# Kernel optimization log

Measured on AMD Instinct MI355X. Metric: run time of the kernel, lower is better.

Reference implementation:

```python
import jax, jax.numpy as jnp
from jax import lax
import numpy as np

B = 8
NUM_ANCHORS = 1047552
PROPOSAL_COUNT = 1000
NMS_THRESHOLD = 0.7
RPN_BBOX_STD_DEV = np.array([0.1, 0.1, 0.2, 0.2], dtype=np.float32)
RPN_NMS_LIMIT = 6000


def setup_inputs() -> dict:
    key = jax.random.key(0)
    k1, k2, k3 = jax.random.split(key, 3)
    rpn_scores = jax.random.uniform(k1, (B, NUM_ANCHORS, 2), dtype=jnp.float32)
    rpn_bbox_delta = jax.random.normal(k2, (B, NUM_ANCHORS, 4), dtype=jnp.float32)
    # Build valid normalized anchors (y1,x1,y2,x2) from uniform randoms.
    u = jax.random.uniform(k3, (NUM_ANCHORS, 4), dtype=jnp.float32)
    cy, cx = u[:, 0], u[:, 1]
    h = u[:, 2] * 0.2 + 0.01
    w = u[:, 3] * 0.2 + 0.01
    anchors = jnp.stack([cy - 0.5 * h, cx - 0.5 * w, cy + 0.5 * h, cx + 0.5 * w], axis=-1)
    anchors = jnp.clip(anchors, 0.0, 1.0)
    return {"rpn_scores": rpn_scores, "rpn_bbox_delta": rpn_bbox_delta, "anchors": anchors}


def _apply_box_deltas(boxes, deltas):
    # boxes: [..., (y1,x1,y2,x2)], deltas: [..., (dy,dx,log(dh),log(dw))]
    h = boxes[..., 2] - boxes[..., 0]
    w = boxes[..., 3] - boxes[..., 1]
    cy = boxes[..., 0] + 0.5 * h + deltas[..., 0] * h
    cx = boxes[..., 1] + 0.5 * w + deltas[..., 1] * w
    h = h * jnp.exp(deltas[..., 2])
    w = w * jnp.exp(deltas[..., 3])
    y1 = cy - 0.5 * h
    x1 = cx - 0.5 * w
    return jnp.stack([y1, x1, y1 + h, x1 + w], axis=-1)


def _nms_indices(boxes):
    # Greedy NMS over boxes already sorted by descending score. boxes: [N,4].
    N = boxes.shape[0]
    areas = (boxes[:, 2] - boxes[:, 0]) * (boxes[:, 3] - boxes[:, 1])

    def body(i, state):
        valid, sel = state
        idx = jnp.argmax(valid)          # first still-valid box = highest score
        has = valid[idx]
        sel = sel.at[i].set(jnp.where(has, idx, -1))
        b = boxes[idx]
        yy1 = jnp.maximum(b[0], boxes[:, 0])
        xx1 = jnp.maximum(b[1], boxes[:, 1])
        yy2 = jnp.minimum(b[2], boxes[:, 2])
        xx2 = jnp.minimum(b[3], boxes[:, 3])
        inter = jnp.maximum(yy2 - yy1, 0.0) * jnp.maximum(xx2 - xx1, 0.0)
        union = areas[idx] + areas - inter
        iou = jnp.where(union > 0, inter / union, 0.0)
        keep = valid & (iou <= NMS_THRESHOLD)
        keep = keep.at[idx].set(False)
        valid = jnp.where(has, keep, valid)
        return valid, sel

    valid0 = jnp.ones((N,), dtype=bool)
    sel0 = jnp.full((PROPOSAL_COUNT,), -1, dtype=jnp.int32)
    _, sel = lax.fori_loop(0, PROPOSAL_COUNT, body, (valid0, sel0))
    return sel


def _nms_single(boxes):
    # boxes: [pre_nms_limit, 4] sorted by score desc -> [proposal_count, 4], zero-padded
    sel = _nms_indices(lax.stop_gradient(boxes))
    props = boxes[jnp.clip(sel, 0)]
    return jnp.where(sel[:, None] >= 0, props, 0.0)


def _forward(rpn_scores, rpn_bbox_delta, anchors):
    scores = rpn_scores[:, :, 1]                                   # [B, A]
    deltas = rpn_bbox_delta * jnp.asarray(RPN_BBOX_STD_DEV)        # [B, A, 4]
    pre_nms_limit = min(RPN_NMS_LIMIT, anchors.shape[0])
    top_scores, ix = lax.top_k(scores, pre_nms_limit)              # [B, pre]
    tgt_deltas = jnp.take_along_axis(deltas, ix[..., None], axis=1)  # [B, pre, 4]
    tgt_anchors = anchors[ix]                                      # [B, pre, 4]
    boxes = _apply_box_deltas(tgt_anchors, tgt_deltas)
    boxes = jnp.clip(boxes, 0.0, 1.0)                              # window (0,0,1,1)
    proposals = jax.vmap(_nms_single)(boxes)                       # [B, proposal_count, 4]
    return proposals


def reference(rpn_scores, rpn_bbox_delta, anchors):
    return _forward(rpn_scores, rpn_bbox_delta, anchors)
```

## Files before the change

### kernel.cpp

```cpp
#include <hip/hip_runtime.h>
#include <stdint.h>

#define NBATCH   8
#define NA       1047552
#define PRE_NMS  6000
#define NPROP    1000
#define BINS     2048
#define HB       64
#define GB       128
#define CAND_CAP 8192
#define NMS_THR  0.7f
#define GBUF     1024
#define SCAP     2048
#define PCHUNK   32
#define PCAP     256
#define REJW     192
#define PTI      64
#define PTJ      1024
#define JR       4

#define OFF_HIST  ((size_t)0)
#define OFF_BOFF  (OFF_HIST + (size_t)NBATCH*HB*BINS*2)
#define OFF_BCNT  (OFF_BOFF + (size_t)NBATCH*BINS*4)
#define OFF_CTR   (OFF_BCNT + (size_t)NBATCH*BINS*4)
#define CTR_BYTES ((size_t)(32 + NBATCH*PCHUNK*4 + NBATCH*BINS*4))
#define OFF_CAND  (OFF_CTR + 66624)
#define OFF_BOXES (OFF_CAND + (size_t)NBATCH*CAND_CAP*8)
#define OFF_PAIRS (OFF_BOXES + (size_t)NBATCH*PRE_NMS*16)
#define WS_NEEDED (OFF_PAIRS + (size_t)NBATCH*PCHUNK*PCAP*4)

__device__ __forceinline__ unsigned score_bin(float s) {
    int b = (int)(s * (float)BINS);
    if (b < 0) b = 0;
    if (b > BINS - 1) b = BINS - 1;
    return (unsigned)b;
}

__global__ __launch_bounds__(256) void k_hist(const float* __restrict__ scores,
                                              uint32_t* __restrict__ bcnt) {
    __shared__ uint32_t lh[BINS];
    const int b = blockIdx.y;
    for (int t = threadIdx.x; t < BINS; t += 256) lh[t] = 0;
    __syncthreads();
    const float4* s4 = reinterpret_cast<const float4*>(scores) + (size_t)b * (NA / 2);
    const int n4 = NA / 2;
    const int stride = gridDim.x * 256;
    for (int i = blockIdx.x * 256 + threadIdx.x; i < n4; i += stride) {
        float4 v = s4[i];
        atomicAdd(&lh[score_bin(v.y)], 1u);
        atomicAdd(&lh[score_bin(v.w)], 1u);
    }
    __syncthreads();
    for (int t = threadIdx.x; t < BINS; t += 256) {
        uint32_t v = lh[t];
        if (v) atomicAdd(&bcnt[(size_t)b * BINS + t], v);
    }
}

__global__ __launch_bounds__(256) void k_thresh2(const uint32_t* __restrict__ bcnt,
                                                 uint32_t* __restrict__ boff,
                                                 uint32_t* __restrict__ cbin) {
    __shared__ uint32_t hsum[BINS];
    __shared__ uint32_t csum[256];
    __shared__ int sC;
    const int b = blockIdx.x;
    const int t = threadIdx.x;
    if (t == 0) sC = 0;
    for (int p = t; p < BINS; p += 256) hsum[p] = bcnt[(size_t)b * BINS + p];
    __syncthreads();
    {
        uint32_t c = 0;
        for (int q = 0; q < 8; ++q) c += hsum[t * 8 + q];
        csum[t] = c;
    }
    __syncthreads();
    if (t == 0) {
        uint32_t suf = 0;
        for (int c = 255; c >= 0; --c) { uint32_t v = csum[c]; csum[c] = suf; suf += v; }
    }
    __syncthreads();
    uint32_t acc = csum[t];
    for (int q = 7; q >= 0; --q) {
        int bin = t * 8 + q;
        uint32_t h = hsum[bin];
        boff[(size_t)b * BINS + bin] = acc;
        if (acc + h >= PRE_NMS) atomicMax(&sC, bin);
        acc += h;
    }
    __syncthreads();
    if (t == 0) cbin[b] = (uint32_t)sC;
}

__global__ __launch_bounds__(256) void k_gather(const float* __restrict__ scores,
                                                const uint32_t* __restrict__ cbin,
                                                const uint32_t* __restrict__ boff,
                                                uint32_t* __restrict__ binpos,
                                                uint64_t* __restrict__ cand) {
    __shared__ uint64_t keybuf[GBUF];
    __shared__ uint16_t binbuf[GBUF];
    __shared__ uint32_t bcnts[BINS];
    __shared__ uint32_t gbase[BINS];
    __shared__ uint32_t nbuf;
    const int b = blockIdx.y;
    const unsigned C = cbin[b];
    for (int t = threadIdx.x; t < BINS; t += 256) bcnts[t] = 0;
    if (threadIdx.x == 0) nbuf = 0;
    __syncthreads();
    const float4* s4 = reinterpret_cast<const float4*>(scores) + (size_t)b * (NA / 2);
    const int n4 = NA / 2;
    const int stride = gridDim.x * 256;
    uint64_t* cb = cand + (size_t)b * CAND_CAP;
    for (int i = blockIdx.x * 256 + threadIdx.x; i < n4; i += stride) {
        float4 v = s4[i];
        float sc[2] = { v.y, v.w };
        #pragma unroll
        for (int h = 0; h < 2; ++h) {
            unsigned bin = score_bin(sc[h]);
            if (bin >= C) {
                unsigned idx = 2u * (unsigned)i + (unsigned)h;
                uint64_t key = ((uint64_t)__float_as_uint(sc[h]) << 32) | (uint32_t)(~idx);
                unsigned p = atomicAdd(&nbuf, 1u);
                if (p < GBUF) {
                    keybuf[p] = key; binbuf[p] = (uint16_t)bin;
                    atomicAdd(&bcnts[bin], 1u);
                } else {
                    unsigned pos = boff[(size_t)b * BINS + bin] +
                                   atomicAdd(&binpos[(size_t)b * BINS + bin], 1u);
                    if (pos < CAND_CAP) cb[pos] = key;
                }
            }
        }
    }
    __syncthreads();
    for (int t = threadIdx.x; t < BINS; t += 256) {
        uint32_t c = bcnts[t];
        if (c) gbase[t] = boff[(size_t)b * BINS + t] +
                          atomicAdd(&binpos[(size_t)b * BINS + t], c);
        bcnts[t] = 0;
    }
    __syncthreads();
    unsigned n = nbuf; if (n > GBUF) n = GBUF;
    for (unsigned p = threadIdx.x; p < n; p += 256) {
        unsigned bn = binbuf[p];
        unsigned pos = gbase[bn] + atomicAdd(&bcnts[bn], 1u);
        if (pos < CAND_CAP) cb[pos] = keybuf[p];
    }
}

__global__ __launch_bounds__(256) void k_binsort(const uint32_t* __restrict__ cbin,
                                                 const uint32_t* __restrict__ boff,
                                                 const uint32_t* __restrict__ bcnt,
                                                 const uint64_t* __restrict__ cand,
                                                 const float* __restrict__ deltas,
                                                 const float* __restrict__ anchors,
                                                 float4* __restrict__ boxesOut) {
    __shared__ uint64_t s[SCAP];
    const int b = blockIdx.y;
    const unsigned bin = cbin[b] + blockIdx.x;
    if (bin >= BINS) return;
    unsigned cnt = bcnt[(size_t)b * BINS + bin];
    if (cnt == 0) return;
    unsigned start = boff[(size_t)b * BINS + bin];
    if (start >= PRE_NMS) return;
    if (start + cnt > CAND_CAP) cnt = CAND_CAP - start;
    if (cnt > SCAP) cnt = SCAP;
    unsigned m = 256;
    while (m < cnt) m <<= 1;
    const uint64_t* seg = cand + (size_t)b * CAND_CAP + start;
    for (unsigned i = threadIdx.x; i < m; i += 256)
        s[i] = (i < cnt) ? ~seg[i] : ~0ull;
    __syncthreads();
    for (unsigned k = 2; k <= m; k <<= 1) {
        for (unsigned j = k >> 1; j > 0; j >>= 1) {
            for (unsigned i = threadIdx.x; i < m; i += 256) {
                unsigned ixj = i ^ j;
                if (ixj > i) {
                    uint64_t a = s[i], c = s[ixj];
                    bool up = ((i & k) == 0);
                    if ((a > c) == up) { s[i] = c; s[ixj] = a; }
                }
            }
            __syncthreads();
        }
    }
    for (unsigned i = threadIdx.x; i < cnt; i += 256) {
        unsigned rank = start + i;
        if (rank >= PRE_NMS) continue;
        unsigned idx = (uint32_t)s[i];
        float4 o = make_float4(0.f, 0.f, 0.f, 0.f);
        if (idx < NA) {
            float4 a = reinterpret_cast<const float4*>(anchors)[idx];
            float4 d = reinterpret_cast<const float4*>(deltas)[(size_t)b * NA + idx];
            float h = a.z - a.x, w = a.w - a.y;
            float cy = a.x + 0.5f * h + (d.x * 0.1f) * h;
            float cx = a.y + 0.5f * w + (d.y * 0.1f) * w;
            h = h * expf(d.z * 0.2f);
            w = w * expf(d.w * 0.2f);
            float y1 = cy - 0.5f * h, x1 = cx - 0.5f * w;
            float y2 = y1 + h,        x2 = x1 + w;
            o.x = fminf(fmaxf(y1, 0.f), 1.f);
            o.y = fminf(fmaxf(x1, 0.f), 1.f);
            o.z = fminf(fmaxf(y2, 0.f), 1.f);
            o.w = fminf(fmaxf(x2, 0.f), 1.f);
        }
        boxesOut[(size_t)b * PRE_NMS + rank] = o;
    }
}

__global__ __launch_bounds__(256) void k_pairs(const float4* __restrict__ boxes,
                                               uint32_t* __restrict__ pcnt,
                                               uint32_t* __restrict__ pairs) {
    const int jb = blockIdx.x;
    const int ib = blockIdx.y;
    const int b  = blockIdx.z;
    const int i0 = ib * PTI;
    const int j0 = jb * PTJ;
    if (i0 > j0 + PTJ - 1) return;
    __shared__ float4 bi[PTI];
    __shared__ float  ai[PTI];
    const int tid = threadIdx.x;
    const float4* bx = boxes + (size_t)b * PRE_NMS;
    const float S = NMS_THR / (1.0f + NMS_THR);
    if (tid < PTI) {
        int ii = i0 + tid;
        float4 v = (ii < PRE_NMS) ? bx[ii] : make_float4(2.f, 2.f, 2.f, 2.f);
        bi[tid] = v;
        ai[tid] = S * ((v.z - v.x) * (v.w - v.y));
    }
    float4 vj[JR]; float aj[JR];
    #pragma unroll
    for (int r = 0; r < JR; ++r) {
        int j = j0 + r * 256 + tid;
        float4 v = (j < PRE_NMS) ? bx[j] : make_float4(2.f, 2.f, 2.f, 2.f);
        vj[r] = v;
        aj[r] = S * ((v.z - v.x) * (v.w - v.y));
    }
    __syncthreads();
    uint32_t* pc = pcnt + b * PCHUNK;
    uint32_t* pb = pairs + (size_t)b * PCHUNK * PCAP;
    const bool touchesDiag = (i0 + PTI - 1 >= j0);
    if (touchesDiag) {
        for (int it = 0; it < PTI; ++it) {
            float4 vi = bi[it];
            float air = ai[it];
            unsigned i = (unsigned)(i0 + it);
            #pragma unroll
            for (int r = 0; r < JR; ++r) {
                float ih = fmaxf(fminf(vj[r].z, vi.z) - fmaxf(vj[r].x, vi.x), 0.f);
                float iw = fmaxf(fminf(vj[r].w, vi.w) - fmaxf(vj[r].y, vi.y), 0.f);
                float inter = ih * iw;
                unsigned j = (unsigned)(j0 + r * 256 + tid);
                if (inter > air + aj[r] && i < j) {
                    unsigned c = j >> 8;
                    unsigned pos = atomicAdd(&pc[c], 1u);
                    if (pos < PCAP) pb[(size_t)c * PCAP + pos] = (j << 13) | i;
                }
            }
        }
    } else {
        #pragma unroll 2
        for (int it = 0; it < PTI; ++it) {
            float4 vi = bi[it];
            float air = ai[it];
            #pragma unroll
            for (int r = 0; r < JR; ++r) {
                float ih = fmaxf(fminf(vj[r].z, vi.z) - fmaxf(vj[r].x, vi.x), 0.f);
                float iw = fmaxf(fminf(vj[r].w, vi.w) - fmaxf(vj[r].y, vi.y), 0.f);
                float inter = ih * iw;
                if (inter > air + aj[r]) {
                    unsigned i = (unsigned)(i0 + it);
                    unsigned j = (unsigned)(j0 + r * 256 + tid);
                    unsigned c = j >> 8;
                    unsigned pos = atomicAdd(&pc[c], 1u);
                    if (pos < PCAP) pb[(size_t)c * PCAP + pos] = (j << 13) | i;
                }
            }
        }
    }
}

__global__ __launch_bounds__(256) void k_nms_emit(const uint32_t* __restrict__ pcnt,
                                                  const uint32_t* __restrict__ pairsIn,
                                                  const float4* __restrict__ boxes,
                                                  float4* __restrict__ out) {
    __shared__ uint32_t sp[PCHUNK * PCAP];
    __shared__ uint32_t cpref[PCHUNK + 1];
    __shared__ uint32_t rejA[REJW], pre[REJW + 1];
    __shared__ uint32_t baseW[8], curW[8], nextW[8];
    __shared__ int changed;
    const int b = blockIdx.x;
    const int tid = threadIdx.x;
    if (tid == 0) {
        unsigned s = 0;
        for (int c = 0; c < PCHUNK; ++c) {
            cpref[c] = s;
            unsigned cc = pcnt[b * PCHUNK + c];
            if (cc > PCAP) cc = PCAP;
            s += cc;
        }
        cpref[PCHUNK] = s;
    }
    for (int t = tid; t < REJW; t += 256) rejA[t] = 0;
    __syncthreads();
    for (int c = 0; c < PCHUNK; ++c) {
        unsigned cnt = cpref[c + 1] - cpref[c];
        for (unsigned k = tid; k < cnt; k += 256)
            sp[cpref[c] + k] = pairsIn[((size_t)b * PCHUNK + c) * PCAP + k];
    }
    __syncthreads();
    const int NCH = (PRE_NMS + 255) >> 8;
    for (int c = 0; c < NCH; ++c) {
        const unsigned lo = cpref[c], hi = cpref[c + 1];
        if (lo == hi) continue;
        if (tid == 0) changed = 0;
        if (tid < 8) baseW[tid] = 0;
        __syncthreads();
        for (unsigned p = lo + tid; p < hi; p += 256) {
            unsigned u = sp[p];
            unsigned j = u >> 13, i = u & 8191u;
            if ((int)(i >> 8) == c) {
                changed = 1;
            } else if (!((rejA[i >> 5] >> (i & 31)) & 1u)) {
                atomicOr(&baseW[(j >> 5) & 7], 1u << (j & 31));
            }
        }
        __syncthreads();
        const int hasIn = changed;
        if (hasIn) {
            if (tid < 8) curW[tid] = baseW[tid];
            __syncthreads();
            for (int it2 = 0; it2 < 256; ++it2) {
                if (tid == 0) changed = 0;
                if (tid < 8) nextW[tid] = baseW[tid];
                __syncthreads();
                for (unsigned p = lo + tid; p < hi; p += 256) {
                    unsigned u = sp[p];
                    unsigned j = u >> 13, i = u & 8191u;
                    if ((int)(i >> 8) == c &&
                        !((curW[(i >> 5) & 7] >> (i & 31)) & 1u))
                        atomicOr(&nextW[(j >> 5) & 7], 1u << (j & 31));
                }
                __syncthreads();
                if (tid < 8) {
                    if (nextW[tid] != curW[tid]) changed = 1;
                    curW[tid] = nextW[tid];
                }
                __syncthreads();
                if (!changed) break;
            }
            if (tid < 8) rejA[c * 8 + tid] = curW[tid];
        } else {
            if (tid < 8) rejA[c * 8 + tid] = baseW[tid];
        }
        __syncthreads();
    }
    if (tid == 0) {
        unsigned c2 = 0;
        for (int w = 0; w < REJW; ++w) { pre[w] = c2; c2 += __popc(rejA[w]); }
        pre[REJW] = c2;
    }
    __syncthreads();
    const float4* bx = boxes + (size_t)b * PRE_NMS;
    float4* ob = out + (size_t)b * NPROP;
    for (int j = tid; j < PRE_NMS; j += 256) {
        unsigned w = (unsigned)j >> 5, bit = (unsigned)j & 31;
        if ((rejA[w] >> bit) & 1u) continue;
        unsigned rank = (unsigned)j - (pre[w] + __popc(rejA[w] & ((1u << bit) - 1u)));
        if (rank < NPROP) ob[rank] = bx[j];
    }
}

extern "C" void kernel_launch(void* const* d_in, const int* in_sizes, int n_in,
                              void* d_out, int out_size, void* d_ws, size_t ws_size,
                              hipStream_t stream) {
    const float* scores  = (const float*)d_in[0];
    const float* deltas  = (const float*)d_in[1];
    const float* anchors = (const float*)d_in[2];

    if (ws_size < WS_NEEDED) return;

    char* ws = (char*)d_ws;
    uint32_t* boff   = (uint32_t*)(ws + OFF_BOFF);
    uint32_t* bcnt   = (uint32_t*)(ws + OFF_BCNT);
    uint32_t* cbin   = (uint32_t*)(ws + OFF_CTR);
    uint32_t* pcnt   = cbin + NBATCH;
    uint32_t* binpos = pcnt + NBATCH * PCHUNK;
    uint64_t* cand   = (uint64_t*)(ws + OFF_CAND);
    float4*   boxes  = (float4*)(ws + OFF_BOXES);
    uint32_t* pairs  = (uint32_t*)(ws + OFF_PAIRS);

    hipMemsetAsync((void*)bcnt, 0, (size_t)NBATCH * BINS * 4 + CTR_BYTES, stream);
    hipMemsetAsync(d_out, 0, (size_t)NBATCH * NPROP * 4 * sizeof(float), stream);

    k_hist   <<<dim3(HB, NBATCH), 256, 0, stream>>>(scores, bcnt);
    k_thresh2<<<NBATCH, 256, 0, stream>>>(bcnt, boff, cbin);
    k_gather <<<dim3(GB, NBATCH), 256, 0, stream>>>(scores, cbin, boff, binpos, cand);
    k_binsort<<<dim3(128, NBATCH), 256, 0, stream>>>(cbin, boff, bcnt, cand,
                                                     deltas, anchors, boxes);
    k_pairs  <<<dim3((PRE_NMS + PTJ - 1) / PTJ, (PRE_NMS + PTI - 1) / PTI, NBATCH),
               256, 0, stream>>>(boxes, pcnt, pairs);
    k_nms_emit<<<NBATCH, 256, 0, stream>>>(pcnt, pairs, boxes, (float4*)d_out);
}
```

Baseline: 402.1 us.

## Fuse candidate prefiltering into histogram pass and merge threshold with gather

The histogram kernel now also stages every score above a fixed prefilter bin into a per-batch workspace buffer. A merged threshold-and-gather kernel then scatters candidates from that small staging buffer, so the second full read of the score array is avoided. If the threshold bin falls below the prefilter bin, it falls back to a single-block full scan. The output memset is replaced by zero-filling the unused tail in the emit kernel. The fixed prefilter bin assumes a score distribution like the test's uniform inputs, and the fallback path would be very slow.

Measured after the change: 434.1 us. +7.9%, slower.

```diff
diff --git a/kernel.cpp b/kernel.cpp
--- a/kernel.cpp
+++ b/kernel.cpp
@@ -7,10 +7,8 @@
 #define NPROP    1000
 #define BINS     2048
 #define HB       64
-#define GB       128
 #define CAND_CAP 8192
 #define NMS_THR  0.7f
-#define GBUF     1024
 #define SCAP     2048
 #define PCHUNK   32
 #define PCAP     256
@@ -18,9 +16,12 @@
 #define PTI      64
 #define PTJ      1024
 #define JR       4
-
-#define OFF_HIST  ((size_t)0)
-#define OFF_BOFF  (OFF_HIST + (size_t)NBATCH*HB*BINS*2)
+#define PREF_BIN 1990u
+#define PSTAGE_CAP 32768u
+#define HBUF     1024
+
+#define OFF_PSTAGE ((size_t)0)
+#define OFF_BOFF  (OFF_PSTAGE + (size_t)NBATCH*PSTAGE_CAP*8)
 #define OFF_BCNT  (OFF_BOFF + (size_t)NBATCH*BINS*4)
 #define OFF_CTR   (OFF_BCNT + (size_t)NBATCH*BINS*4)
 #define CTR_BYTES ((size_t)(32 + NBATCH*PCHUNK*4 + NBATCH*BINS*4))
@@ -37,113 +38,120 @@
 }
 
 __global__ __launch_bounds__(256) void k_hist(const float* __restrict__ scores,
-                                              uint32_t* __restrict__ bcnt) {
+                                              uint32_t* __restrict__ bcnt,
+                                              uint64_t* __restrict__ pstage,
+                                              uint32_t* __restrict__ pn) {
     __shared__ uint32_t lh[BINS];
+    __shared__ uint64_t kb[HBUF];
+    __shared__ uint32_t nbuf, sbase;
     const int b = blockIdx.y;
     for (int t = threadIdx.x; t < BINS; t += 256) lh[t] = 0;
+    if (threadIdx.x == 0) nbuf = 0;
     __syncthreads();
     const float4* s4 = reinterpret_cast<const float4*>(scores) + (size_t)b * (NA / 2);
     const int n4 = NA / 2;
     const int stride = gridDim.x * 256;
-    for (int i = blockIdx.x * 256 + threadIdx.x; i < n4; i += stride) {
-        float4 v = s4[i];
-        atomicAdd(&lh[score_bin(v.y)], 1u);
-        atomicAdd(&lh[score_bin(v.w)], 1u);
-    }
-    __syncthreads();
-    for (int t = threadIdx.x; t < BINS; t += 256) {
-        uint32_t v = lh[t];
-        if (v) atomicAdd(&bcnt[(size_t)b * BINS + t], v);
-    }
-}
-
-__global__ __launch_bounds__(256) void k_thresh2(const uint32_t* __restrict__ bcnt,
-                                                 uint32_t* __restrict__ boff,
-                                                 uint32_t* __restrict__ cbin) {
-    __shared__ uint32_t hsum[BINS];
-    __shared__ uint32_t csum[256];
-    __shared__ int sC;
-    const int b = blockIdx.x;
-    const int t = threadIdx.x;
-    if (t == 0) sC = 0;
-    for (int p = t; p < BINS; p += 256) hsum[p] = bcnt[(size_t)b * BINS + p];
-    __syncthreads();
-    {
-        uint32_t c = 0;
-        for (int q = 0; q < 8; ++q) c += hsum[t * 8 + q];
-        csum[t] = c;
-    }
-    __syncthreads();
-    if (t == 0) {
-        uint32_t suf = 0;
-        for (int c = 255; c >= 0; --c) { uint32_t v = csum[c]; csum[c] = suf; suf += v; }
-    }
-    __syncthreads();
-    uint32_t acc = csum[t];
-    for (int q = 7; q >= 0; --q) {
-        int bin = t * 8 + q;
-        uint32_t h = hsum[bin];
-        boff[(size_t)b * BINS + bin] = acc;
-        if (acc + h >= PRE_NMS) atomicMax(&sC, bin);
-        acc += h;
-    }
-    __syncthreads();
-    if (t == 0) cbin[b] = (uint32_t)sC;
-}
-
-__global__ __launch_bounds__(256) void k_gather(const float* __restrict__ scores,
-                                                const uint32_t* __restrict__ cbin,
-                                                const uint32_t* __restrict__ boff,
-                                                uint32_t* __restrict__ binpos,
-                                                uint64_t* __restrict__ cand) {
-    __shared__ uint64_t keybuf[GBUF];
-    __shared__ uint16_t binbuf[GBUF];
-    __shared__ uint32_t bcnts[BINS];
-    __shared__ uint32_t gbase[BINS];
-    __shared__ uint32_t nbuf;
-    const int b = blockIdx.y;
-    const unsigned C = cbin[b];
-    for (int t = threadIdx.x; t < BINS; t += 256) bcnts[t] = 0;
-    if (threadIdx.x == 0) nbuf = 0;
-    __syncthreads();
-    const float4* s4 = reinterpret_cast<const float4*>(scores) + (size_t)b * (NA / 2);
-    const int n4 = NA / 2;
-    const int stride = gridDim.x * 256;
-    uint64_t* cb = cand + (size_t)b * CAND_CAP;
+    uint64_t* ps = pstage + (size_t)b * PSTAGE_CAP;
     for (int i = blockIdx.x * 256 + threadIdx.x; i < n4; i += stride) {
         float4 v = s4[i];
         float sc[2] = { v.y, v.w };
         #pragma unroll
         for (int h = 0; h < 2; ++h) {
             unsigned bin = score_bin(sc[h]);
-            if (bin >= C) {
+            atomicAdd(&lh[bin], 1u);
+            if (bin >= PREF_BIN) {
                 unsigned idx = 2u * (unsigned)i + (unsigned)h;
                 uint64_t key = ((uint64_t)__float_as_uint(sc[h]) << 32) | (uint32_t)(~idx);
                 unsigned p = atomicAdd(&nbuf, 1u);
-                if (p < GBUF) {
-                    keybuf[p] = key; binbuf[p] = (uint16_t)bin;
-                    atomicAdd(&bcnts[bin], 1u);
-                } else {
-                    unsigned pos = boff[(size_t)b * BINS + bin] +
-                                   atomicAdd(&binpos[(size_t)b * BINS + bin], 1u);
+                if (p < HBUF) kb[p] = key;
+                else {
+                    unsigned g = atomicAdd(&pn[b], 1u);
+                    if (g < PSTAGE_CAP) ps[g] = key;
+                }
+            }
+        }
+    }
+    __syncthreads();
+    for (int t = threadIdx.x; t < BINS; t += 256) {
+        uint32_t v = lh[t];
+        if (v) atomicAdd(&bcnt[(size_t)b * BINS + t], v);
+    }
+    unsigned n = nbuf; if (n > HBUF) n = HBUF;
+    if (threadIdx.x == 0) sbase = atomicAdd(&pn[b], n);
+    __syncthreads();
+    for (unsigned p = threadIdx.x; p < n; p += 256) {
+        unsigned g = sbase + p;
+        if (g < PSTAGE_CAP) ps[g] = kb[p];
+    }
+}
+
+__global__ __launch_bounds__(256) void k_threshgather(const uint32_t* __restrict__ bcnt,
+                                                      const float* __restrict__ scores,
+                                                      const uint64_t* __restrict__ pstage,
+                                                      const uint32_t* __restrict__ pn,
+                                                      uint32_t* __restrict__ boffG,
+                                                      uint32_t* __restrict__ cbin,
+                                                      uint64_t* __restrict__ cand) {
+    __shared__ uint32_t boffL[BINS];
+    __shared__ uint32_t bposL[BINS];
+    __shared__ uint32_t csum[256];
+    __shared__ int sC;
+    const int b = blockIdx.x;
+    const int t = threadIdx.x;
+    if (t == 0) sC = 0;
+    uint32_t h[8];
+    {
+        uint32_t c = 0;
+        #pragma unroll
+        for (int q = 0; q < 8; ++q) { h[q] = bcnt[(size_t)b * BINS + t * 8 + q]; c += h[q]; }
+        csum[t] = c;
+    }
+    __syncthreads();
+    if (t == 0) {
+        uint32_t suf = 0;
+        for (int c = 255; c >= 0; --c) { uint32_t v = csum[c]; csum[c] = suf; suf += v; }
+    }
+    __syncthreads();
+    uint32_t acc = csum[t];
+    for (int q = 7; q >= 0; --q) {
+        int bin = t * 8 + q;
+        boffL[bin] = acc;
+        bposL[bin] = 0;
+        boffG[(size_t)b * BINS + bin] = acc;
+        if (acc + h[q] >= PRE_NMS) atomicMax(&sC, bin);
+        acc += h[q];
+    }
+    __syncthreads();
+    const unsigned C = (unsigned)sC;
+    if (t == 0) cbin[b] = C;
+    const unsigned n = pn[b];
+    uint64_t* cb = cand + (size_t)b * CAND_CAP;
+    if (n <= PSTAGE_CAP && C >= PREF_BIN) {
+        const uint64_t* ps = pstage + (size_t)b * PSTAGE_CAP;
+        for (unsigned p = t; p < n; p += 256) {
+            uint64_t key = ps[p];
+            unsigned bin = score_bin(__uint_as_float((uint32_t)(key >> 32)));
+            if (bin >= C) {
+                unsigned pos = boffL[bin] + atomicAdd(&bposL[bin], 1u);
+                if (pos < CAND_CAP) cb[pos] = key;
+            }
+        }
+    } else {
+        const float4* s4 = reinterpret_cast<const float4*>(scores) + (size_t)b * (NA / 2);
+        for (int i = t; i < NA / 2; i += 256) {
+            float4 v = s4[i];
+            float sc[2] = { v.y, v.w };
+            #pragma unroll
+            for (int hh = 0; hh < 2; ++hh) {
+                unsigned bin = score_bin(sc[hh]);
+                if (bin >= C) {
+                    unsigned idx = 2u * (unsigned)i + (unsigned)hh;
+                    uint64_t key = ((uint64_t)__float_as_uint(sc[hh]) << 32) | (uint32_t)(~idx);
+                    unsigned pos = boffL[bin] + atomicAdd(&bposL[bin], 1u);
                     if (pos < CAND_CAP) cb[pos] = key;
                 }
             }
         }
-    }
-    __syncthreads();
-    for (int t = threadIdx.x; t < BINS; t += 256) {
-        uint32_t c = bcnts[t];
-        if (c) gbase[t] = boff[(size_t)b * BINS + t] +
-                          atomicAdd(&binpos[(size_t)b * BINS + t], c);
-        bcnts[t] = 0;
-    }
-    __syncthreads();
-    unsigned n = nbuf; if (n > GBUF) n = GBUF;
-    for (unsigned p = threadIdx.x; p < n; p += 256) {
-        unsigned bn = binbuf[p];
-        unsigned pos = gbase[bn] + atomicAdd(&bcnts[bn], 1u);
-        if (pos < CAND_CAP) cb[pos] = keybuf[p];
     }
 }
 
@@ -368,6 +376,9 @@
         unsigned rank = (unsigned)j - (pre[w] + __popc(rejA[w] & ((1u << bit) - 1u)));
         if (rank < NPROP) ob[rank] = bx[j];
     }
+    const unsigned kept = (unsigned)PRE_NMS - pre[REJW];
+    for (unsigned r = kept + tid; r < NPROP; r += 256)
+        ob[r] = make_float4(0.f, 0.f, 0.f, 0.f);
 }
 
 extern "C" void kernel_launch(void* const* d_in, const int* in_sizes, int n_in,
@@ -380,24 +391,23 @@
     if (ws_size < WS_NEEDED) return;
 
     char* ws = (char*)d_ws;
+    uint64_t* pstage = (uint64_t*)(ws + OFF_PSTAGE);
     uint32_t* boff   = (uint32_t*)(ws + OFF_BOFF);
     uint32_t* bcnt   = (uint32_t*)(ws + OFF_BCNT);
     uint32_t* cbin   = (uint32_t*)(ws + OFF_CTR);
     uint32_t* pcnt   = cbin + NBATCH;
-    uint32_t* binpos = pcnt + NBATCH * PCHUNK;
+    uint32_t* pn     = pcnt + NBATCH * PCHUNK;
     uint64_t* cand   = (uint64_t*)(ws + OFF_CAND);
     float4*   boxes  = (float4*)(ws + OFF_BOXES);
     uint32_t* pairs  = (uint32_t*)(ws + OFF_PAIRS);
 
     hipMemsetAsync((void*)bcnt, 0, (size_t)NBATCH * BINS * 4 + CTR_BYTES, stream);
-    hipMemsetAsync(d_out, 0, (size_t)NBATCH * NPROP * 4 * sizeof(float), stream);
-
-    k_hist   <<<dim3(HB, NBATCH), 256, 0, stream>>>(scores, bcnt);
-    k_thresh2<<<NBATCH, 256, 0, stream>>>(bcnt, boff, cbin);
-    k_gather <<<dim3(GB, NBATCH), 256, 0, stream>>>(scores, cbin, boff, binpos, cand);
-    k_binsort<<<dim3(128, NBATCH), 256, 0, stream>>>(cbin, boff, bcnt, cand,
-                                                     deltas, anchors, boxes);
-    k_pairs  <<<dim3((PRE_NMS + PTJ - 1) / PTJ, (PRE_NMS + PTI - 1) / PTI, NBATCH),
-               256, 0, stream>>>(boxes, pcnt, pairs);
-    k_nms_emit<<<NBATCH, 256, 0, stream>>>(pcnt, pairs, boxes, (float4*)d_out);
-}
+
+    k_hist        <<<dim3(HB, NBATCH), 256, 0, stream>>>(scores, bcnt, pstage, pn);
+    k_threshgather<<<NBATCH, 256, 0, stream>>>(bcnt, scores, pstage, pn, boff, cbin, cand);
+    k_binsort     <<<dim3(128, NBATCH), 256, 0, stream>>>(cbin, boff, bcnt, cand,
+                                                          deltas, anchors, boxes);
+    k_pairs       <<<dim3((PRE_NMS + PTJ - 1) / PTJ, (PRE_NMS + PTI - 1) / PTI, NBATCH),
+                    256, 0, stream>>>(boxes, pcnt, pairs);
+    k_nms_emit    <<<NBATCH, 256, 0, stream>>>(pcnt, pairs, boxes, (float4*)d_out);
+}
```
